# Kernel tuning notes

Hardware: AMD Instinct MI355X
Metric: run time of the kernel (lower is better)

Reference implementation:

```python
import jax, jax.numpy as jnp
from jax import lax
import numpy as np

BATCH, T, IN_DIM, RES = 32, 2048, 64, 1024
SPECTRAL_RADIUS, SPARSITY, INPUT_SCALING, LEAK = 1.2, 0.2, 0.5, 0.3


def setup_inputs() -> dict:
    key = jax.random.key(0)
    inputs = jax.random.normal(key, (BATCH, T, IN_DIM), dtype=jnp.float32)
    # Replicate the layer's build(): fixed random reservoir, seeded numpy RNG.
    rng = np.random.RandomState(42)
    W_in = rng.uniform(-INPUT_SCALING, INPUT_SCALING, size=(IN_DIM, RES)).astype(np.float32)
    W_res = rng.randn(RES, RES)
    mask = rng.rand(RES, RES) < SPARSITY
    W_res *= mask
    sr = np.max(np.abs(np.linalg.eigvals(W_res)))
    if sr > 0:
        W_res *= SPECTRAL_RADIUS / sr
    return {
        "inputs": inputs,
        "W_in": jnp.asarray(W_in),
        "W_res": jnp.asarray(W_res.astype(np.float32)),
    }


def reference(inputs, W_in, W_res):
    # inputs: [B, T, I]; W_in: [I, R]; W_res: [R, R]
    leak = jnp.asarray(LEAK, inputs.dtype)
    # Hoist the input projection out of the recurrence (same math, one big GEMM).
    x_proj = jnp.einsum("bti,ir->btr", inputs, W_in)  # [B, T, R]
    state0 = jnp.zeros((inputs.shape[0], W_res.shape[0]), dtype=inputs.dtype)

    def step(state, x_t):  # x_t: [B, R]
        new_state = jnp.tanh(x_t + state @ W_res)
        state = (1.0 - leak) * state + leak * new_state
        return state, state

    _, states = lax.scan(step, state0, jnp.swapaxes(x_proj, 0, 1))  # [T, B, R]
    return jnp.swapaxes(states, 0, 1)  # [B, T, R] (return_sequences=True)
```

## Files before the change

### kernel.cpp

```cpp
#include <hip/hip_runtime.h>

#define T_STEPS 2048
#define NBATCH  32
#define IN_DIM  64
#define RES     1024
#define LEAKF   0.3f
#define NCG     64
#define NBG     4

typedef unsigned long long u64cp;

__global__ __launch_bounds__(256, 1) void esn_persist(
    const float* __restrict__ inp,
    const float* __restrict__ Win,
    const float* __restrict__ Wres,
    float* __restrict__ out,
    float* __restrict__ sT,
    unsigned* __restrict__ flags)
{
    const int tid   = threadIdx.x;
    const int c_loc = tid & 15;
    const int ks    = tid >> 4;
    const int cg    = blockIdx.x;
    const int bg    = blockIdx.y;
    const int c0    = cg * 16;
    const int b0    = bg * 8;
    const int c     = c0 + c_loc;

    float w[64];
    {
        const float* wp = Wres + (size_t)(ks * 64) * RES + c;
        #pragma unroll
        for (int j = 0; j < 64; ++j) w[j] = wp[(size_t)j * RES];
    }

    __shared__ float pl[16][8][17];
    unsigned* flg = flags + bg * NCG;

    const int fb = tid >> 4;
    float s_prev = 0.f;

    for (int t = 0; t < T_STEPS; ++t) {
        float* sTr = sT + ((t & 1) ^ 1) * (RES * NBATCH);
        float* sTw = sT + (t & 1) * (RES * NBATCH);

        float x = 0.f;
        if (tid < 128) {
            const float* inb = inp + ((size_t)(b0 + fb) * T_STEPS + t) * IN_DIM;
            #pragma unroll 8
            for (int i = 0; i < IN_DIM; ++i)
                x = fmaf(inb[i], Win[(size_t)i * RES + c], x);
        }

        if (t > 0) {
            if (tid < NCG) {
                const unsigned tgt = (unsigned)t;
                while (__hip_atomic_load(&flg[tid], __ATOMIC_RELAXED,
                                         __HIP_MEMORY_SCOPE_AGENT) < tgt) { }
            }
            __syncthreads();
        }

        float acc0 = 0.f, acc1 = 0.f, acc2 = 0.f, acc3 = 0.f;
        float acc4 = 0.f, acc5 = 0.f, acc6 = 0.f, acc7 = 0.f;
        if (t > 0) {
            float* sp = sTr + (size_t)(ks * 64) * NBATCH + b0;
            #pragma unroll
            for (int j = 0; j < 64; ++j) {
                u64cp p01 = __hip_atomic_load((u64cp*)(sp + (size_t)j * NBATCH + 0),
                                              __ATOMIC_RELAXED, __HIP_MEMORY_SCOPE_AGENT);
                u64cp p23 = __hip_atomic_load((u64cp*)(sp + (size_t)j * NBATCH + 2),
                                              __ATOMIC_RELAXED, __HIP_MEMORY_SCOPE_AGENT);
                u64cp p45 = __hip_atomic_load((u64cp*)(sp + (size_t)j * NBATCH + 4),
                                              __ATOMIC_RELAXED, __HIP_MEMORY_SCOPE_AGENT);
                u64cp p67 = __hip_atomic_load((u64cp*)(sp + (size_t)j * NBATCH + 6),
                                              __ATOMIC_RELAXED, __HIP_MEMORY_SCOPE_AGENT);
                const float wj = w[j];
                acc0 = fmaf(__uint_as_float((unsigned)(p01       )), wj, acc0);
                acc1 = fmaf(__uint_as_float((unsigned)(p01 >> 32u)), wj, acc1);
                acc2 = fmaf(__uint_as_float((unsigned)(p23       )), wj, acc2);
                acc3 = fmaf(__uint_as_float((unsigned)(p23 >> 32u)), wj, acc3);
                acc4 = fmaf(__uint_as_float((unsigned)(p45       )), wj, acc4);
                acc5 = fmaf(__uint_as_float((unsigned)(p45 >> 32u)), wj, acc5);
                acc6 = fmaf(__uint_as_float((unsigned)(p67       )), wj, acc6);
                acc7 = fmaf(__uint_as_float((unsigned)(p67 >> 32u)), wj, acc7);
            }
        }

        pl[ks][0][c_loc] = acc0;
        pl[ks][1][c_loc] = acc1;
        pl[ks][2][c_loc] = acc2;
        pl[ks][3][c_loc] = acc3;
        pl[ks][4][c_loc] = acc4;
        pl[ks][5][c_loc] = acc5;
        pl[ks][6][c_loc] = acc6;
        pl[ks][7][c_loc] = acc7;
        __syncthreads();

        if (tid < 128) {
            float sum = 0.f;
            #pragma unroll
            for (int q = 0; q < 16; ++q) sum += pl[q][fb][c_loc];

            const float nw = tanhf(x + sum);
            const float sn = fmaf(1.0f - LEAKF, s_prev, LEAKF * nw);
            s_prev = sn;

            out[((size_t)(b0 + fb) * T_STEPS + t) * RES + c] = sn;
            __hip_atomic_store(sTw + (size_t)c * NBATCH + (b0 + fb), sn,
                               __ATOMIC_RELAXED, __HIP_MEMORY_SCOPE_AGENT);
        }
        __syncthreads();

        if (tid == 0)
            __hip_atomic_store(&flg[cg], (unsigned)(t + 1),
                               __ATOMIC_RELAXED, __HIP_MEMORY_SCOPE_AGENT);
    }
}

__global__ __launch_bounds__(256) void esn_step(
    const float* __restrict__ inp,
    const float* __restrict__ Win,
    const float* __restrict__ Wres,
    float* __restrict__ out,
    float* __restrict__ sT,
    int t)
{
    const int tid   = threadIdx.x;
    const int c_loc = tid & 15;
    const int ks    = tid >> 4;
    const int c0    = blockIdx.x * 16;
    const int b0    = blockIdx.y * 8;
    const int c     = c0 + c_loc;

    const float* sTr = sT + ((t & 1) ^ 1) * (RES * NBATCH);
    float*       sTw = sT + (t & 1) * (RES * NBATCH);

    float acc0 = 0.f, acc1 = 0.f, acc2 = 0.f, acc3 = 0.f;
    float acc4 = 0.f, acc5 = 0.f, acc6 = 0.f, acc7 = 0.f;

    if (t > 0) {
        const int kbeg = ks * 64;
        const float* wp = Wres + (size_t)kbeg * RES + c;
        const float* sp = sTr + kbeg * NBATCH + b0;
        #pragma unroll 4
        for (int j = 0; j < 64; ++j) {
            const float w = wp[(size_t)j * RES];
            const float4 sa = *reinterpret_cast<const float4*>(sp + j * NBATCH);
            const float4 sb = *reinterpret_cast<const float4*>(sp + j * NBATCH + 4);
            acc0 = fmaf(sa.x, w, acc0);
            acc1 = fmaf(sa.y, w, acc1);
            acc2 = fmaf(sa.z, w, acc2);
            acc3 = fmaf(sa.w, w, acc3);
            acc4 = fmaf(sb.x, w, acc4);
            acc5 = fmaf(sb.y, w, acc5);
            acc6 = fmaf(sb.z, w, acc6);
            acc7 = fmaf(sb.w, w, acc7);
        }
    }

    __shared__ float pl[16][8][17];
    pl[ks][0][c_loc] = acc0;
    pl[ks][1][c_loc] = acc1;
    pl[ks][2][c_loc] = acc2;
    pl[ks][3][c_loc] = acc3;
    pl[ks][4][c_loc] = acc4;
    pl[ks][5][c_loc] = acc5;
    pl[ks][6][c_loc] = acc6;
    pl[ks][7][c_loc] = acc7;
    __syncthreads();

    if (tid < 128) {
        const int b  = tid >> 4;
        const int cl = tid & 15;
        const int cg = c0 + cl;
        const int bg = b0 + b;

        float sum = 0.f;
        #pragma unroll
        for (int q = 0; q < 16; ++q) sum += pl[q][b][cl];

        const float* inb = inp + ((size_t)bg * T_STEPS + t) * IN_DIM;
        float x = 0.f;
        #pragma unroll 8
        for (int i = 0; i < IN_DIM; ++i)
            x = fmaf(inb[i], Win[(size_t)i * RES + cg], x);

        const float a  = x + sum;
        const float nw = tanhf(a);
        const float spv = (t > 0) ? sTr[cg * NBATCH + bg] : 0.f;
        const float sn = fmaf(1.0f - LEAKF, spv, LEAKF * nw);

        out[((size_t)bg * T_STEPS + t) * RES + cg] = sn;
        sTw[cg * NBATCH + bg] = sn;
    }
}

extern "C" void kernel_launch(void* const* d_in, const int* in_sizes, int n_in,
                              void* d_out, int out_size, void* d_ws, size_t ws_size,
                              hipStream_t stream)
{
    const float* inp  = (const float*)d_in[0];
    const float* Win  = (const float*)d_in[1];
    const float* Wres = (const float*)d_in[2];
    float* out = (float*)d_out;
    float* sT  = (float*)d_ws;

    const size_t stateBytes = (size_t)2 * RES * NBATCH * sizeof(float);
    const size_t flagBytes  = (size_t)NBG * NCG * sizeof(unsigned);

    if (ws_size >= stateBytes + flagBytes) {
        unsigned* flags = (unsigned*)((char*)d_ws + stateBytes);
        hipMemsetAsync(flags, 0, flagBytes, stream);
        hipLaunchKernelGGL(esn_persist, dim3(NCG, NBG), dim3(256), 0, stream,
                           inp, Win, Wres, out, sT, flags);
        return;
    }

    dim3 grid(64, 4), blk(256);
    for (int t = 0; t < T_STEPS; ++t) {
        hipLaunchKernelGGL(esn_step, grid, blk, 0, stream,
                           inp, Win, Wres, out, sT, t);
    }
}
```

Measured before the change: 20.23 ms.

## Stage per-batch-group state into padded LDS before reservoir matvec

Each block now loads its batch group's full previous state (1024x8 floats) cooperatively from global into padded shared memory once per step, then runs the matvec from LDS instead of every thread issuing its own atomic global loads. The state buffer is re-laid out per batch group ([bg][2][RES][8]) so the copy-in is contiguous. The input projection loads are also vectorised with float4. This adds an extra syncthreads and roughly 33KB of LDS per block, and the copy-in sits on the critical path of each timestep.

```diff
diff --git a/kernel.cpp b/kernel.cpp
--- a/kernel.cpp
+++ b/kernel.cpp
@@ -15,7 +15,7 @@
     const float* __restrict__ Win,
     const float* __restrict__ Wres,
     float* __restrict__ out,
-    float* __restrict__ sT,
+    float* __restrict__ sC,
     unsigned* __restrict__ flags)
 {
     const int tid   = threadIdx.x;
@@ -34,22 +34,30 @@
         for (int j = 0; j < 64; ++j) w[j] = wp[(size_t)j * RES];
     }
 
+    __shared__ __align__(16) float sst[8256];
     __shared__ float pl[16][8][17];
+
     unsigned* flg = flags + bg * NCG;
+    float* sCb = sC + (size_t)bg * 2 * RES * 8;
 
     const int fb = tid >> 4;
     float s_prev = 0.f;
 
     for (int t = 0; t < T_STEPS; ++t) {
-        float* sTr = sT + ((t & 1) ^ 1) * (RES * NBATCH);
-        float* sTw = sT + (t & 1) * (RES * NBATCH);
+        float* sCr = sCb + ((t & 1) ^ 1) * (RES * 8);
+        float* sCw = sCb + (t & 1) * (RES * 8);
 
         float x = 0.f;
         if (tid < 128) {
             const float* inb = inp + ((size_t)(b0 + fb) * T_STEPS + t) * IN_DIM;
-            #pragma unroll 8
-            for (int i = 0; i < IN_DIM; ++i)
-                x = fmaf(inb[i], Win[(size_t)i * RES + c], x);
+            #pragma unroll
+            for (int i = 0; i < IN_DIM; i += 4) {
+                const float4 v = *reinterpret_cast<const float4*>(inb + i);
+                x = fmaf(v.x, Win[(size_t)(i + 0) * RES + c], x);
+                x = fmaf(v.y, Win[(size_t)(i + 1) * RES + c], x);
+                x = fmaf(v.z, Win[(size_t)(i + 2) * RES + c], x);
+                x = fmaf(v.w, Win[(size_t)(i + 3) * RES + c], x);
+            }
         }
 
         if (t > 0) {
@@ -59,31 +67,40 @@
                                          __HIP_MEMORY_SCOPE_AGENT) < tgt) { }
             }
             __syncthreads();
+
+            #pragma unroll
+            for (int i = 0; i < 8; ++i) {
+                const int m = i * 256 + tid;
+                u64cp lo = __hip_atomic_load((u64cp*)(sCr + (size_t)m * 4),
+                                             __ATOMIC_RELAXED, __HIP_MEMORY_SCOPE_AGENT);
+                u64cp hi = __hip_atomic_load((u64cp*)(sCr + (size_t)m * 4 + 2),
+                                             __ATOMIC_RELAXED, __HIP_MEMORY_SCOPE_AGENT);
+                float4* dst = (float4*)((char*)sst + (size_t)m * 16 + (m >> 7) * 16);
+                *dst = make_float4(__uint_as_float((unsigned)(lo       )),
+                                   __uint_as_float((unsigned)(lo >> 32u)),
+                                   __uint_as_float((unsigned)(hi       )),
+                                   __uint_as_float((unsigned)(hi >> 32u)));
+            }
+            __syncthreads();
         }
 
         float acc0 = 0.f, acc1 = 0.f, acc2 = 0.f, acc3 = 0.f;
         float acc4 = 0.f, acc5 = 0.f, acc6 = 0.f, acc7 = 0.f;
         if (t > 0) {
-            float* sp = sTr + (size_t)(ks * 64) * NBATCH + b0;
+            const char* base = (const char*)sst + (size_t)(ks * 64) * 32 + ks * 16;
             #pragma unroll
             for (int j = 0; j < 64; ++j) {
-                u64cp p01 = __hip_atomic_load((u64cp*)(sp + (size_t)j * NBATCH + 0),
-                                              __ATOMIC_RELAXED, __HIP_MEMORY_SCOPE_AGENT);
-                u64cp p23 = __hip_atomic_load((u64cp*)(sp + (size_t)j * NBATCH + 2),
-                                              __ATOMIC_RELAXED, __HIP_MEMORY_SCOPE_AGENT);
-                u64cp p45 = __hip_atomic_load((u64cp*)(sp + (size_t)j * NBATCH + 4),
-                                              __ATOMIC_RELAXED, __HIP_MEMORY_SCOPE_AGENT);
-                u64cp p67 = __hip_atomic_load((u64cp*)(sp + (size_t)j * NBATCH + 6),
-                                              __ATOMIC_RELAXED, __HIP_MEMORY_SCOPE_AGENT);
+                const float4 sa = *reinterpret_cast<const float4*>(base + j * 32);
+                const float4 sb = *reinterpret_cast<const float4*>(base + j * 32 + 16);
                 const float wj = w[j];
-                acc0 = fmaf(__uint_as_float((unsigned)(p01       )), wj, acc0);
-                acc1 = fmaf(__uint_as_float((unsigned)(p01 >> 32u)), wj, acc1);
-                acc2 = fmaf(__uint_as_float((unsigned)(p23       )), wj, acc2);
-                acc3 = fmaf(__uint_as_float((unsigned)(p23 >> 32u)), wj, acc3);
-                acc4 = fmaf(__uint_as_float((unsigned)(p45       )), wj, acc4);
-                acc5 = fmaf(__uint_as_float((unsigned)(p45 >> 32u)), wj, acc5);
-                acc6 = fmaf(__uint_as_float((unsigned)(p67       )), wj, acc6);
-                acc7 = fmaf(__uint_as_float((unsigned)(p67 >> 32u)), wj, acc7);
+                acc0 = fmaf(sa.x, wj, acc0);
+                acc1 = fmaf(sa.y, wj, acc1);
+                acc2 = fmaf(sa.z, wj, acc2);
+                acc3 = fmaf(sa.w, wj, acc3);
+                acc4 = fmaf(sb.x, wj, acc4);
+                acc5 = fmaf(sb.y, wj, acc5);
+                acc6 = fmaf(sb.z, wj, acc6);
+                acc7 = fmaf(sb.w, wj, acc7);
             }
         }
 
@@ -107,7 +124,7 @@
             s_prev = sn;
 
             out[((size_t)(b0 + fb) * T_STEPS + t) * RES + c] = sn;
-            __hip_atomic_store(sTw + (size_t)c * NBATCH + (b0 + fb), sn,
+            __hip_atomic_store(sCw + (size_t)c * 8 + fb, sn,
                                __ATOMIC_RELAXED, __HIP_MEMORY_SCOPE_AGENT);
         }
         __syncthreads();
@@ -173,26 +190,26 @@
     if (tid < 128) {
         const int b  = tid >> 4;
         const int cl = tid & 15;
-        const int cg = c0 + cl;
-        const int bg = b0 + b;
+        const int cgl = c0 + cl;
+        const int bgl = b0 + b;
 
         float sum = 0.f;
         #pragma unroll
         for (int q = 0; q < 16; ++q) sum += pl[q][b][cl];
 
-        const float* inb = inp + ((size_t)bg * T_STEPS + t) * IN_DIM;
+        const float* inb = inp + ((size_t)bgl * T_STEPS + t) * IN_DIM;
         float x = 0.f;
         #pragma unroll 8
         for (int i = 0; i < IN_DIM; ++i)
-            x = fmaf(inb[i], Win[(size_t)i * RES + cg], x);
+            x = fmaf(inb[i], Win[(size_t)i * RES + cgl], x);
 
         const float a  = x + sum;
         const float nw = tanhf(a);
-        const float spv = (t > 0) ? sTr[cg * NBATCH + bg] : 0.f;
+        const float spv = (t > 0) ? sTr[cgl * NBATCH + bgl] : 0.f;
         const float sn = fmaf(1.0f - LEAKF, spv, LEAKF * nw);
 
-        out[((size_t)bg * T_STEPS + t) * RES + cg] = sn;
-        sTw[cg * NBATCH + bg] = sn;
+        out[((size_t)bgl * T_STEPS + t) * RES + cgl] = sn;
+        sTw[cgl * NBATCH + bgl] = sn;
     }
 }
 
@@ -204,19 +221,20 @@
     const float* Win  = (const float*)d_in[1];
     const float* Wres = (const float*)d_in[2];
     float* out = (float*)d_out;
-    float* sT  = (float*)d_ws;
-
-    const size_t stateBytes = (size_t)2 * RES * NBATCH * sizeof(float);
+
+    const size_t stateBytes = (size_t)NBG * 2 * RES * 8 * sizeof(float);
     const size_t flagBytes  = (size_t)NBG * NCG * sizeof(unsigned);
 
     if (ws_size >= stateBytes + flagBytes) {
+        float* sC = (float*)d_ws;
         unsigned* flags = (unsigned*)((char*)d_ws + stateBytes);
         hipMemsetAsync(flags, 0, flagBytes, stream);
         hipLaunchKernelGGL(esn_persist, dim3(NCG, NBG), dim3(256), 0, stream,
-                           inp, Win, Wres, out, sT, flags);
+                           inp, Win, Wres, out, sC, flags);
         return;
     }
 
+    float* sT = (float*)d_ws;
     dim3 grid(64, 4), blk(256);
     for (int t = 0; t < T_STEPS; ++t) {
         hipLaunchKernelGGL(esn_step, grid, blk, 0, stream,
```

Result: slower. 21.18 ms (+4.7%).
